# Optimization experiments

Hardware: AMD Instinct MI355X
Metric: run time of the kernel (lower is better)

## Reference

```python
import jax, jax.numpy as jnp
import numpy as np

EPS = 1e-08
NUM_EMBEDDINGS = 8192
EMBEDDING_DIM = 256
N_TOKENS = 32768


def setup_inputs() -> dict:
    key = jax.random.key(0)
    k1, k2, k3 = jax.random.split(key, 3)
    input_data = jax.random.normal(k1, (N_TOKENS, EMBEDDING_DIM), dtype=jnp.float32)
    rand = jax.random.normal(k2, (N_TOKENS, EMBEDDING_DIM), dtype=jnp.float32)
    codebooks = jax.random.normal(k3, (NUM_EMBEDDINGS, EMBEDDING_DIM), dtype=jnp.float32)
    return {"input_data": input_data, "rand": rand, "codebooks": codebooks}


def reference(input_data, rand, codebooks):
    # d2: (N, K) -- this full matrix is what a fused kernel would avoid.
    d2 = (jnp.sum(input_data * input_data, axis=1, keepdims=True)
          - 2.0 * input_data @ codebooks.T
          + jnp.sum(codebooks * codebooks, axis=1)[None, :])
    min_idx = jnp.argmin(d2, axis=1)                      # (N,)
    hard_q = codebooks[min_idx]                           # (N, D)

    # Noise substitution: scale unit-ish gaussian noise to the residual norm.
    r_norm = jnp.linalg.norm(input_data - hard_q, axis=1, keepdims=True)
    n_norm = jnp.linalg.norm(rand, axis=1, keepdims=True)
    quantized_input = input_data + (r_norm / (n_norm + EPS)) * rand

    # Perplexity from codebook usage counts (no grad path in original).
    counts = jnp.zeros((NUM_EMBEDDINGS,), dtype=jnp.float32).at[min_idx].add(1.0)
    total = jnp.maximum(counts.sum(), 1.0)
    avg_probs = counts / total
    perplexity = jnp.exp(-jnp.sum(avg_probs * jnp.log(avg_probs + EPS)))
    num_unique_indices = jnp.sum(counts > 0).astype(jnp.int32)
    return quantized_input, perplexity, num_unique_indices
```

## Files before the change

kernel.cpp:

```cpp
#include <hip/hip_runtime.h>
#include <stdint.h>

#define N_TOKENS 32768
#define N_CODES  8192
#define DIM      256
#define EPSF     1e-8f

typedef __bf16 bf16x8 __attribute__((ext_vector_type(8)));
typedef float  f32x4  __attribute__((ext_vector_type(4)));

#define WS_CNORM_OFF  (4u*1024u*1024u)
#define WS_MAXV_OFF   (WS_CNORM_OFF + N_CODES*4u)
#define WS_HIST_OFF   (WS_MAXV_OFF + N_TOKENS*4u)

__global__ __launch_bounds__(256) void k_prep(const float* __restrict__ cbf,
                                              unsigned short* __restrict__ cbh,
                                              float* __restrict__ cnorm,
                                              int* __restrict__ hist) {
    const int tid = blockIdx.x * 256 + threadIdx.x;
    if (tid < N_CODES) hist[tid] = 0;

    const int w = threadIdx.x >> 6;
    const int lane = threadIdx.x & 63;
    const int row = blockIdx.x * 4 + w;

    const float4 v = ((const float4*)(cbf + (size_t)row * DIM))[lane];
    float sq = v.x * v.x + v.y * v.y + v.z * v.z + v.w * v.w;

    ushort4 u;
    u.x = __builtin_bit_cast(unsigned short, (__bf16)v.x);
    u.y = __builtin_bit_cast(unsigned short, (__bf16)v.y);
    u.z = __builtin_bit_cast(unsigned short, (__bf16)v.z);
    u.w = __builtin_bit_cast(unsigned short, (__bf16)v.w);
    ((ushort4*)(cbh + (size_t)row * DIM))[lane] = u;

    #pragma unroll
    for (int d = 1; d < 64; d <<= 1) sq += __shfl_xor(sq, d);
    if (lane == 0) cnorm[row] = sq;
}

__global__ __launch_bounds__(256, 2) void k_argmin(const float* __restrict__ X,
                                                   const unsigned short* __restrict__ cbh,
                                                   const float* __restrict__ cnorm,
                                                   float* __restrict__ maxvOut,
                                                   int* __restrict__ hist) {
    __shared__ __attribute__((aligned(16))) char Bs[2][32768];
    __shared__ __attribute__((aligned(16))) float cnS[2][4][64];
    __shared__ float redv[4][64];
    __shared__ int   redi[4][64];

    const int tid  = threadIdx.x;
    const int w    = tid >> 6;
    const int lane = tid & 63;
    const int lr   = lane & 15;
    const int lq   = lane >> 4;
    const int r0   = blockIdx.x * 64;
    const int mycol = w * 16 + lr;

    {
        const float4* Xf4 = (const float4*)(X + (size_t)(r0 + 16 * w) * DIM);
        #pragma unroll
        for (int i = 0; i < 16; ++i) {
            const float4 v = Xf4[i * 64 + lane];
            ushort4 u;
            u.x = __builtin_bit_cast(unsigned short, (__bf16)v.x);
            u.y = __builtin_bit_cast(unsigned short, (__bf16)v.y);
            u.z = __builtin_bit_cast(unsigned short, (__bf16)v.z);
            u.w = __builtin_bit_cast(unsigned short, (__bf16)v.w);
            *(ushort4*)(&Bs[0][0] + (16 * w + i) * 544 + lane * 8) = u;
        }
    }
    __syncthreads();

    bf16x8 A[4][8];
    #pragma unroll
    for (int mf = 0; mf < 4; ++mf)
        #pragma unroll
        for (int kc = 0; kc < 8; ++kc)
            A[mf][kc] = *(const bf16x8*)(&Bs[0][0] + (mf * 16 + lr) * 544 + kc * 64 + lq * 16);
    __syncthreads();

    const int half = lane >> 5, l5 = lane & 31;
    int srcoff[8];
    #pragma unroll
    for (int s = 0; s < 8; ++s) {
        const int c = w * 16 + 2 * s + half;
        const int j = (l5 - c) & 31;
        srcoff[s] = c * 512 + j * 16;
    }
    const char* cbb = (const char*)cbh;

    #pragma unroll
    for (int s = 0; s < 8; ++s)
        __builtin_amdgcn_global_load_lds(
            (const __attribute__((address_space(1))) unsigned int*)(cbb + srcoff[s]),
            (__attribute__((address_space(3))) unsigned int*)(&Bs[0][w * 8192 + s * 1024]),
            16, 0, 0);
    __builtin_amdgcn_global_load_lds(
        (const __attribute__((address_space(1))) unsigned int*)(cnorm + lane),
        (__attribute__((address_space(3))) unsigned int*)(&cnS[0][w][0]),
        4, 0, 0);

    float maxv[16];
    int   maxi[16];
    #pragma unroll
    for (int i = 0; i < 16; ++i) { maxv[i] = -3.4e38f; maxi[i] = 0; }

    for (int cc = 0; cc < 128; ++cc) {
        asm volatile("s_waitcnt vmcnt(0)" ::: "memory");

        if (cc + 1 < 128) {
            const char* src = cbb + (size_t)(cc + 1) * 32768;
            char* dst = &Bs[(cc + 1) & 1][w * 8192];
            #pragma unroll
            for (int s = 0; s < 8; ++s)
                __builtin_amdgcn_global_load_lds(
                    (const __attribute__((address_space(1))) unsigned int*)(src + srcoff[s]),
                    (__attribute__((address_space(3))) unsigned int*)(dst + s * 1024),
                    16, 0, 0);
            __builtin_amdgcn_global_load_lds(
                (const __attribute__((address_space(1))) unsigned int*)(cnorm + (cc + 1) * 64 + lane),
                (__attribute__((address_space(3))) unsigned int*)(&cnS[(cc + 1) & 1][w][0]),
                4, 0, 0);
        }

        const float cinit = -0.5f * cnS[cc & 1][w][mycol];
        f32x4 acc[4];
        #pragma unroll
        for (int mf = 0; mf < 4; ++mf) {
            acc[mf][0] = cinit; acc[mf][1] = cinit; acc[mf][2] = cinit; acc[mf][3] = cinit;
        }

        const char* bp = &Bs[cc & 1][0] + mycol * 512;
        #pragma unroll
        for (int kc = 0; kc < 8; ++kc) {
            const bf16x8 b = *(const bf16x8*)(bp + (((kc * 4 + lq + mycol) & 31) << 4));
            #pragma unroll
            for (int mf = 0; mf < 4; ++mf)
                acc[mf] = __builtin_amdgcn_mfma_f32_16x16x32_bf16(A[mf][kc], b, acc[mf], 0, 0, 0);
        }

        const int col = cc * 64 + mycol;
        #pragma unroll
        for (int mf = 0; mf < 4; ++mf)
            #pragma unroll
            for (int r = 0; r < 4; ++r) {
                const float v = acc[mf][r];
                const int j = mf * 4 + r;
                if (v > maxv[j]) { maxv[j] = v; maxi[j] = col; }
            }
    }

    #pragma unroll
    for (int mf = 0; mf < 4; ++mf)
        #pragma unroll
        for (int r = 0; r < 4; ++r) {
            float v = maxv[mf * 4 + r]; int ix = maxi[mf * 4 + r];
            #pragma unroll
            for (int d = 1; d <= 8; d <<= 1) {
                const float ov = __shfl_xor(v, d);
                const int   oi = __shfl_xor(ix, d);
                if (ov > v || (ov == v && oi < ix)) { v = ov; ix = oi; }
            }
            if (lr == 0) {
                const int row = mf * 16 + lq * 4 + r;
                redv[w][row] = v; redi[w][row] = ix;
            }
        }
    __syncthreads();

    if (tid < 64) {
        float v = redv[0][tid]; int ix = redi[0][tid];
        #pragma unroll
        for (int ww = 1; ww < 4; ++ww) {
            const float ov = redv[ww][tid]; const int oi = redi[ww][tid];
            if (ov > v || (ov == v && oi < ix)) { v = ov; ix = oi; }
        }
        maxvOut[r0 + tid] = v;
        atomicAdd(&hist[ix], 1);
    }
}

__global__ __launch_bounds__(256) void k_quant(const float* __restrict__ X,
                                               const float* __restrict__ R,
                                               const float* __restrict__ Mv,
                                               float* __restrict__ out) {
    const int w = threadIdx.x >> 6;
    const int lane = threadIdx.x & 63;
    const int tok = blockIdx.x * 4 + w;

    const float4 x = ((const float4*)(X + (size_t)tok * DIM))[lane];
    const float4 r = ((const float4*)(R + (size_t)tok * DIM))[lane];

    float x2 = x.x * x.x + x.y * x.y + x.z * x.z + x.w * x.w;
    float n2 = r.x * r.x + r.y * r.y + r.z * r.z + r.w * r.w;
    #pragma unroll
    for (int d = 1; d < 64; d <<= 1) {
        x2 += __shfl_xor(x2, d);
        n2 += __shfl_xor(n2, d);
    }
    const float mv = Mv[tok];
    const float d2 = fmaxf(fmaf(-2.f, mv, x2), 0.f);
    const float s = sqrtf(d2) / (sqrtf(n2) + EPSF);

    float4 o;
    o.x = fmaf(s, r.x, x.x);
    o.y = fmaf(s, r.y, x.y);
    o.z = fmaf(s, r.z, x.z);
    o.w = fmaf(s, r.w, x.w);
    ((float4*)(out + (size_t)tok * DIM))[lane] = o;
}

__global__ __launch_bounds__(256) void k_stats(const int* __restrict__ hist,
                                               float* __restrict__ outs) {
    float s = 0.f; int u = 0;
    for (int b = threadIdx.x; b < N_CODES; b += 256) {
        const float c = (float)hist[b];
        if (c > 0.f) ++u;
        const float p = c * (1.f / (float)N_TOKENS);
        s += p * logf(p + EPSF);
    }
    #pragma unroll
    for (int d = 1; d < 64; d <<= 1) {
        s += __shfl_xor(s, d);
        u += __shfl_xor(u, d);
    }
    __shared__ float ss[4];
    __shared__ int   su[4];
    const int w = threadIdx.x >> 6, lane = threadIdx.x & 63;
    if (lane == 0) { ss[w] = s; su[w] = u; }
    __syncthreads();
    if (threadIdx.x == 0) {
        const float st = ss[0] + ss[1] + ss[2] + ss[3];
        const int ut = su[0] + su[1] + su[2] + su[3];
        outs[0] = expf(-st);
        outs[1] = (float)ut;
    }
}

extern "C" void kernel_launch(void* const* d_in, const int* in_sizes, int n_in,
                              void* d_out, int out_size, void* d_ws, size_t ws_size,
                              hipStream_t stream) {
    const float* X = (const float*)d_in[0];
    const float* R = (const float*)d_in[1];
    const float* C = (const float*)d_in[2];
    float* out = (float*)d_out;

    char* ws = (char*)d_ws;
    unsigned short* cbh = (unsigned short*)ws;
    float* cnorm = (float*)(ws + WS_CNORM_OFF);
    float* maxv  = (float*)(ws + WS_MAXV_OFF);
    int*   hist  = (int*)(ws + WS_HIST_OFF);

    k_prep  <<<N_CODES / 4,  256, 0, stream>>>(C, cbh, cnorm, hist);
    k_argmin<<<N_TOKENS / 64, 256, 0, stream>>>(X, cbh, cnorm, maxv, hist);
    k_quant <<<N_TOKENS / 4, 256, 0, stream>>>(X, R, maxv, out);
    k_stats <<<1, 256, 0, stream>>>(hist, out + (size_t)N_TOKENS * DIM);
}
```

Before: 262.4 us.

## Share codebook tiles across two row groups and fuse quantize epilogue into argmin

The argmin kernel now uses 512 threads covering 128 tokens, so each codebook tile loaded into LDS serves two 64-row groups of waves. This halves the codebook traffic per token and removes the separate quantize kernel and its maxv round-trip through global memory. The cost is a block-wide barrier every iteration in place of the per-wave vmcnt wait, plus larger LDS use and fewer blocks (256), which may hurt occupancy and latency hiding. The stats kernel is widened to 1024 threads.

```diff
diff --git a/kernel.cpp b/kernel.cpp
--- a/kernel.cpp
+++ b/kernel.cpp
@@ -10,8 +10,7 @@
 typedef float  f32x4  __attribute__((ext_vector_type(4)));
 
 #define WS_CNORM_OFF  (4u*1024u*1024u)
-#define WS_MAXV_OFF   (WS_CNORM_OFF + N_CODES*4u)
-#define WS_HIST_OFF   (WS_MAXV_OFF + N_TOKENS*4u)
+#define WS_HIST_OFF   (WS_CNORM_OFF + N_CODES*4u)
 
 __global__ __launch_bounds__(256) void k_prep(const float* __restrict__ cbf,
                                               unsigned short* __restrict__ cbh,
@@ -39,23 +38,27 @@
     if (lane == 0) cnorm[row] = sq;
 }
 
-__global__ __launch_bounds__(256, 2) void k_argmin(const float* __restrict__ X,
+__global__ __launch_bounds__(512, 2) void k_argmin(const float* __restrict__ X,
+                                                   const float* __restrict__ R,
                                                    const unsigned short* __restrict__ cbh,
                                                    const float* __restrict__ cnorm,
-                                                   float* __restrict__ maxvOut,
+                                                   float* __restrict__ out,
                                                    int* __restrict__ hist) {
-    __shared__ __attribute__((aligned(16))) char Bs[2][32768];
-    __shared__ __attribute__((aligned(16))) float cnS[2][4][64];
-    __shared__ float redv[4][64];
-    __shared__ int   redi[4][64];
+    __shared__ __attribute__((aligned(16))) char smem[87040];
+    float* cnS   = (float*)(smem + 65536);
+    float* redv  = (float*)(smem + 66048);
+    int*   redi  = (int*)(smem + 68096);
+    float* maxvS = (float*)(smem + 70144);
 
     const int tid  = threadIdx.x;
     const int w    = tid >> 6;
     const int lane = tid & 63;
     const int lr   = lane & 15;
     const int lq   = lane >> 4;
-    const int r0   = blockIdx.x * 64;
-    const int mycol = w * 16 + lr;
+    const int th   = w >> 2;
+    const int wc   = w & 3;
+    const int r0   = blockIdx.x * 128;
+    const int mycol = wc * 16 + lr;
 
     {
         const float4* Xf4 = (const float4*)(X + (size_t)(r0 + 16 * w) * DIM);
@@ -67,7 +70,7 @@
             u.y = __builtin_bit_cast(unsigned short, (__bf16)v.y);
             u.z = __builtin_bit_cast(unsigned short, (__bf16)v.z);
             u.w = __builtin_bit_cast(unsigned short, (__bf16)v.w);
-            *(ushort4*)(&Bs[0][0] + (16 * w + i) * 544 + lane * 8) = u;
+            *(ushort4*)(smem + (16 * w + i) * 544 + lane * 8) = u;
         }
     }
     __syncthreads();
@@ -77,29 +80,31 @@
     for (int mf = 0; mf < 4; ++mf)
         #pragma unroll
         for (int kc = 0; kc < 8; ++kc)
-            A[mf][kc] = *(const bf16x8*)(&Bs[0][0] + (mf * 16 + lr) * 544 + kc * 64 + lq * 16);
+            A[mf][kc] = *(const bf16x8*)(smem + (64 * th + mf * 16 + lr) * 544 + kc * 64 + lq * 16);
     __syncthreads();
 
     const int half = lane >> 5, l5 = lane & 31;
-    int srcoff[8];
-    #pragma unroll
-    for (int s = 0; s < 8; ++s) {
-        const int c = w * 16 + 2 * s + half;
+    int srcoff[4];
+    #pragma unroll
+    for (int s = 0; s < 4; ++s) {
+        const int c = 8 * w + 2 * s + half;
         const int j = (l5 - c) & 31;
         srcoff[s] = c * 512 + j * 16;
     }
     const char* cbb = (const char*)cbh;
 
     #pragma unroll
-    for (int s = 0; s < 8; ++s)
+    for (int s = 0; s < 4; ++s)
         __builtin_amdgcn_global_load_lds(
             (const __attribute__((address_space(1))) unsigned int*)(cbb + srcoff[s]),
-            (__attribute__((address_space(3))) unsigned int*)(&Bs[0][w * 8192 + s * 1024]),
+            (__attribute__((address_space(3))) unsigned int*)(smem + w * 4096 + s * 1024),
             16, 0, 0);
-    __builtin_amdgcn_global_load_lds(
-        (const __attribute__((address_space(1))) unsigned int*)(cnorm + lane),
-        (__attribute__((address_space(3))) unsigned int*)(&cnS[0][w][0]),
-        4, 0, 0);
+    if (w == 0)
+        __builtin_amdgcn_global_load_lds(
+            (const __attribute__((address_space(1))) unsigned int*)(cnorm + lane),
+            (__attribute__((address_space(3))) unsigned int*)(cnS),
+            4, 0, 0);
+    __syncthreads();
 
     float maxv[16];
     int   maxi[16];
@@ -107,34 +112,34 @@
     for (int i = 0; i < 16; ++i) { maxv[i] = -3.4e38f; maxi[i] = 0; }
 
     for (int cc = 0; cc < 128; ++cc) {
-        asm volatile("s_waitcnt vmcnt(0)" ::: "memory");
-
+        const int cur = (cc & 1) * 32768;
         if (cc + 1 < 128) {
+            const int nxt = ((cc + 1) & 1) * 32768;
             const char* src = cbb + (size_t)(cc + 1) * 32768;
-            char* dst = &Bs[(cc + 1) & 1][w * 8192];
-            #pragma unroll
-            for (int s = 0; s < 8; ++s)
+            #pragma unroll
+            for (int s = 0; s < 4; ++s)
                 __builtin_amdgcn_global_load_lds(
                     (const __attribute__((address_space(1))) unsigned int*)(src + srcoff[s]),
-                    (__attribute__((address_space(3))) unsigned int*)(dst + s * 1024),
+                    (__attribute__((address_space(3))) unsigned int*)(smem + nxt + w * 4096 + s * 1024),
                     16, 0, 0);
-            __builtin_amdgcn_global_load_lds(
-                (const __attribute__((address_space(1))) unsigned int*)(cnorm + (cc + 1) * 64 + lane),
-                (__attribute__((address_space(3))) unsigned int*)(&cnS[(cc + 1) & 1][w][0]),
-                4, 0, 0);
-        }
-
-        const float cinit = -0.5f * cnS[cc & 1][w][mycol];
+            if (w == 0)
+                __builtin_amdgcn_global_load_lds(
+                    (const __attribute__((address_space(1))) unsigned int*)(cnorm + (cc + 1) * 64 + lane),
+                    (__attribute__((address_space(3))) unsigned int*)(cnS + ((cc + 1) & 1) * 64),
+                    4, 0, 0);
+        }
+
+        const float cinit = -0.5f * cnS[(cc & 1) * 64 + mycol];
         f32x4 acc[4];
         #pragma unroll
         for (int mf = 0; mf < 4; ++mf) {
             acc[mf][0] = cinit; acc[mf][1] = cinit; acc[mf][2] = cinit; acc[mf][3] = cinit;
         }
 
-        const char* bp = &Bs[cc & 1][0] + mycol * 512;
         #pragma unroll
         for (int kc = 0; kc < 8; ++kc) {
-            const bf16x8 b = *(const bf16x8*)(bp + (((kc * 4 + lq + mycol) & 31) << 4));
+            const bf16x8 b = *(const bf16x8*)(smem + cur + mycol * 512 +
+                                              (((kc * 4 + lq + mycol) & 31) << 4));
             #pragma unroll
             for (int mf = 0; mf < 4; ++mf)
                 acc[mf] = __builtin_amdgcn_mfma_f32_16x16x32_bf16(A[mf][kc], b, acc[mf], 0, 0, 0);
@@ -149,6 +154,8 @@
                 const int j = mf * 4 + r;
                 if (v > maxv[j]) { maxv[j] = v; maxi[j] = col; }
             }
+
+        __syncthreads();
     }
 
     #pragma unroll
@@ -164,57 +171,55 @@
             }
             if (lr == 0) {
                 const int row = mf * 16 + lq * 4 + r;
-                redv[w][row] = v; redi[w][row] = ix;
+                redv[w * 64 + row] = v; redi[w * 64 + row] = ix;
             }
         }
     __syncthreads();
 
-    if (tid < 64) {
-        float v = redv[0][tid]; int ix = redi[0][tid];
+    if (tid < 128) {
+        const int t = tid, tth = t >> 6, tl = t & 63;
+        float v = redv[(4 * tth) * 64 + tl]; int ix = redi[(4 * tth) * 64 + tl];
         #pragma unroll
         for (int ww = 1; ww < 4; ++ww) {
-            const float ov = redv[ww][tid]; const int oi = redi[ww][tid];
+            const float ov = redv[(4 * tth + ww) * 64 + tl];
+            const int   oi = redi[(4 * tth + ww) * 64 + tl];
             if (ov > v || (ov == v && oi < ix)) { v = ov; ix = oi; }
         }
-        maxvOut[r0 + tid] = v;
+        maxvS[t] = v;
         atomicAdd(&hist[ix], 1);
     }
-}
-
-__global__ __launch_bounds__(256) void k_quant(const float* __restrict__ X,
-                                               const float* __restrict__ R,
-                                               const float* __restrict__ Mv,
-                                               float* __restrict__ out) {
-    const int w = threadIdx.x >> 6;
-    const int lane = threadIdx.x & 63;
-    const int tok = blockIdx.x * 4 + w;
-
-    const float4 x = ((const float4*)(X + (size_t)tok * DIM))[lane];
-    const float4 r = ((const float4*)(R + (size_t)tok * DIM))[lane];
-
-    float x2 = x.x * x.x + x.y * x.y + x.z * x.z + x.w * x.w;
-    float n2 = r.x * r.x + r.y * r.y + r.z * r.z + r.w * r.w;
-    #pragma unroll
-    for (int d = 1; d < 64; d <<= 1) {
-        x2 += __shfl_xor(x2, d);
-        n2 += __shfl_xor(n2, d);
-    }
-    const float mv = Mv[tok];
-    const float d2 = fmaxf(fmaf(-2.f, mv, x2), 0.f);
-    const float s = sqrtf(d2) / (sqrtf(n2) + EPSF);
-
-    float4 o;
-    o.x = fmaf(s, r.x, x.x);
-    o.y = fmaf(s, r.y, x.y);
-    o.z = fmaf(s, r.z, x.z);
-    o.w = fmaf(s, r.w, x.w);
-    ((float4*)(out + (size_t)tok * DIM))[lane] = o;
-}
-
-__global__ __launch_bounds__(256) void k_stats(const int* __restrict__ hist,
-                                               float* __restrict__ outs) {
+    __syncthreads();
+
+    for (int i = 0; i < 16; ++i) {
+        const int tl = 16 * w + i;
+        const int tok = r0 + tl;
+        const float4 x = ((const float4*)(X + (size_t)tok * DIM))[lane];
+        const float4 r = ((const float4*)(R + (size_t)tok * DIM))[lane];
+
+        float x2 = x.x * x.x + x.y * x.y + x.z * x.z + x.w * x.w;
+        float n2 = r.x * r.x + r.y * r.y + r.z * r.z + r.w * r.w;
+        #pragma unroll
+        for (int d = 1; d < 64; d <<= 1) {
+            x2 += __shfl_xor(x2, d);
+            n2 += __shfl_xor(n2, d);
+        }
+        const float mv = maxvS[tl];
+        const float d2 = fmaxf(fmaf(-2.f, mv, x2), 0.f);
+        const float s = sqrtf(d2) / (sqrtf(n2) + EPSF);
+
+        float4 o;
+        o.x = fmaf(s, r.x, x.x);
+        o.y = fmaf(s, r.y, x.y);
+        o.z = fmaf(s, r.z, x.z);
+        o.w = fmaf(s, r.w, x.w);
+        ((float4*)(out + (size_t)tok * DIM))[lane] = o;
+    }
+}
+
+__global__ __launch_bounds__(1024) void k_stats(const int* __restrict__ hist,
+                                                float* __restrict__ outs) {
     float s = 0.f; int u = 0;
-    for (int b = threadIdx.x; b < N_CODES; b += 256) {
+    for (int b = threadIdx.x; b < N_CODES; b += 1024) {
         const float c = (float)hist[b];
         if (c > 0.f) ++u;
         const float p = c * (1.f / (float)N_TOKENS);
@@ -225,14 +230,15 @@
         s += __shfl_xor(s, d);
         u += __shfl_xor(u, d);
     }
-    __shared__ float ss[4];
-    __shared__ int   su[4];
+    __shared__ float ss[16];
+    __shared__ int   su[16];
     const int w = threadIdx.x >> 6, lane = threadIdx.x & 63;
     if (lane == 0) { ss[w] = s; su[w] = u; }
     __syncthreads();
     if (threadIdx.x == 0) {
-        const float st = ss[0] + ss[1] + ss[2] + ss[3];
-        const int ut = su[0] + su[1] + su[2] + su[3];
+        float st = 0.f; int ut = 0;
+        #pragma unroll
+        for (int i = 0; i < 16; ++i) { st += ss[i]; ut += su[i]; }
         outs[0] = expf(-st);
         outs[1] = (float)ut;
     }
@@ -249,11 +255,9 @@
     char* ws = (char*)d_ws;
     unsigned short* cbh = (unsigned short*)ws;
     float* cnorm = (float*)(ws + WS_CNORM_OFF);
-    float* maxv  = (float*)(ws + WS_MAXV_OFF);
     int*   hist  = (int*)(ws + WS_HIST_OFF);
 
-    k_prep  <<<N_CODES / 4,  256, 0, stream>>>(C, cbh, cnorm, hist);
-    k_argmin<<<N_TOKENS / 64, 256, 0, stream>>>(X, cbh, cnorm, maxv, hist);
-    k_quant <<<N_TOKENS / 4, 256, 0, stream>>>(X, R, maxv, out);
-    k_stats <<<1, 256, 0, stream>>>(hist, out + (size_t)N_TOKENS * DIM);
-}
+    k_prep  <<<N_CODES / 4,    256, 0, stream>>>(C, cbh, cnorm, hist);
+    k_argmin<<<N_TOKENS / 128, 512, 0, stream>>>(X, R, cbh, cnorm, out, hist);
+    k_stats <<<1, 1024, 0, stream>>>(hist, out + (size_t)N_TOKENS * DIM);
+}
```

Result: faster. 244.8 us (-6.7%).
